# Performance work log

Hardware: AMD Instinct MI355X
Metric: run time of the kernel (lower is better)

## Reference

```python
import jax, jax.numpy as jnp
import numpy as np

BN_EPS = 1e-5

def setup_inputs() -> dict:
    key = jax.random.key(0)
    k0, k1, k2, k3, k4 = jax.random.split(key, 5)
    B, N, D, E = 8, 256, 128, 4096
    x_l = jax.random.normal(k0, (B, N, D), dtype=jnp.float32)
    src = jax.random.randint(k1, (E,), 0, N)
    dst = jax.random.randint(k2, (E,), 0, N)
    edge_index_l = jnp.stack([src, dst], axis=0)  # [2, E]
    mask_l = jax.random.randint(k3, (B, N), 0, 2).astype(bool)
    W = jax.random.normal(k4, (D, D), dtype=jnp.float32) * (1.0 / np.sqrt(D))
    b = jnp.zeros((D,), jnp.float32)
    gamma = jnp.ones((D,), jnp.float32)
    beta = jnp.zeros((D,), jnp.float32)
    return {"x_l": x_l, "edge_index_l": edge_index_l, "mask_l": mask_l,
            "W": W, "b": b, "gamma": gamma, "beta": beta}


def reference(x_l, edge_index_l, mask_l, W, b, gamma, beta):
    # x_l: [B, N, D]; edge_index_l: [2, E]; mask_l: [B, N] bool
    B, N, D = x_l.shape
    src, dst = edge_index_l[0], edge_index_l[1]
    # Vectorized replacement of the Python edge loop: edges with dst - src == 3
    # zero the mask at both endpoints (the explicit interaction zeroing in the
    # original is subsumed by the mask, since masked entries never survive).
    cov = (dst - src) == 3  # [E] bool
    hit = jnp.zeros((N,), bool)
    hit = hit.at[src].max(cov)
    hit = hit.at[dst].max(cov)
    mask = mask_l & ~hit[None, :]  # [B, N]
    # Pairwise mask: outer AND minus diagonal
    eye = jnp.eye(N, dtype=bool)
    pair_mask = (mask[:, :, None] & mask[:, None, :]) & ~eye[None]  # [B, N, N]
    # Outer-product interaction: [B, N, N, D]
    interaction = x_l[:, :, None, :] * x_l[:, None, :, :]
    # Linear
    h = jnp.einsum('bijd,ed->bije', interaction, W) + b
    # BatchNorm1d over the masked (selected) rows, training-mode batch stats.
    m = pair_mask[..., None].astype(h.dtype)  # [B, N, N, 1]
    cnt = jnp.maximum(jnp.sum(m), 1.0)
    mean = jnp.sum(h * m, axis=(0, 1, 2)) / cnt  # [D]
    var = jnp.sum(m * (h - mean) ** 2, axis=(0, 1, 2)) / cnt  # biased, as torch BN
    hn = (h - mean) * jax.lax.rsqrt(var + BN_EPS) * gamma + beta
    # Dropout is identity in eval mode; LeakyReLU slope 0.01 (torch default).
    out = jax.nn.leaky_relu(hn, negative_slope=0.01) * m  # zero non-selected entries
    return out, pair_mask
```

## Files before the change

### kernel.cpp

```cpp
#include <hip/hip_runtime.h>

#define B_ 8
#define N_ 256
#define D_ 128
#define E_ 4096

typedef __attribute__((ext_vector_type(8))) short bf16x8;
typedef __attribute__((ext_vector_type(4))) float f32x4;
typedef __attribute__((ext_vector_type(2))) float f32x2;

__device__ inline unsigned int pack2bf(float lo, float hi) {
    unsigned ul = __float_as_uint(lo);
    ul = ul + 0x7FFFu + ((ul >> 16) & 1u);
    unsigned uh = __float_as_uint(hi);
    uh = uh + 0x7FFFu + ((uh >> 16) & 1u);
    return (ul >> 16) | (uh & 0xFFFF0000u);
}

__device__ inline unsigned short f2bf(float f) {
    unsigned u = __float_as_uint(f);
    u = u + 0x7FFFu + ((u >> 16) & 1u);
    return (unsigned short)(u >> 16);
}


__global__ __launch_bounds__(256) void k_prep(const void* __restrict__ edges_raw,
                                              const void* __restrict__ mask_raw,
                                              const float* __restrict__ W,
                                              int* __restrict__ mask,
                                              int* __restrict__ jlist,
                                              int* __restrict__ jcnt,
                                              unsigned short* __restrict__ Wb,
                                              float* __restrict__ Wt,
                                              float* __restrict__ tq,
                                              float* __restrict__ dq) {
    int blk = blockIdx.x, tid = threadIdx.x;
    if (blk >= B_) {
        int idx = (blk - B_) * 256 + tid;
        if (idx < 16384) {
            float w = W[idx];
            Wb[idx] = f2bf(w);
            int e = idx >> 7, d = idx & 127;
            Wt[d * D_ + e] = w;
        } else if (idx < 16512) tq[idx - 16384] = 0.0f;
        else dq[idx - 16512] = 0.0f;
        return;
    }
    int b = blk;
    __shared__ unsigned char hit[N_];
    __shared__ int flags[2];
    __shared__ int wcnt[4], wbase[4];
    hit[tid] = 0;
    if (tid < 2) flags[tid] = 0;
    __syncthreads();

    const unsigned char* mb = (const unsigned char*)mask_raw;
    int loc_m = 0;
    for (int idx = tid; idx < B_ * N_; idx += 256)
        if ((idx & 3) && mb[idx]) loc_m = 1;
    if (loc_m) flags[0] = 1;
    const int* e32 = (const int*)edges_raw;
    int loc_e = 0;
    for (int idx = tid; idx < 2 * E_; idx += 256)
        if ((idx & 1) && e32[idx]) loc_e = 1;
    if (loc_e) flags[1] = 1;
    __syncthreads();

    int mask_is_u8 = flags[0], e_is_i32 = flags[1];
    const long long* e64 = (const long long*)edges_raw;
    for (int e = tid; e < E_; e += 256) {
        int s, d;
        if (e_is_i32) { s = e32[e]; d = e32[E_ + e]; }
        else          { s = (int)e64[e]; d = (int)e64[E_ + e]; }
        if (d - s == 3) { hit[s] = 1; hit[d] = 1; }
    }
    __syncthreads();

    const int* m32 = (const int*)mask_raw;
    int lane = tid & 63, wid = tid >> 6;
    int raw = mask_is_u8 ? (int)(mb[b * N_ + tid] != 0) : (int)(m32[b * N_ + tid] != 0);
    int m = raw && (hit[tid] == 0);
    mask[b * N_ + tid] = m;
    unsigned long long bal = __ballot(m);
    if (lane == 0) wcnt[wid] = __popcll(bal);
    __syncthreads();
    if (tid == 0) {
        int base = 0;
        for (int w = 0; w < 4; ++w) { wbase[w] = base; base += wcnt[w]; }
        jcnt[b] = base;
    }
    __syncthreads();
    if (m) {
        int pos = wbase[wid] + __popcll(bal & ((1ull << lane) - 1ull));
        jlist[b * N_ + pos] = tid;
    }
}

__global__ __launch_bounds__(128) void k_gram3(const float* __restrict__ x,
                                               const int* __restrict__ jlist,
                                               const int* __restrict__ jcnt,
                                               float* __restrict__ part,
                                               float* __restrict__ s1,
                                               float* __restrict__ cdiag) {
    int d = blockIdx.x, b = blockIdx.y, dp = threadIdx.x;
    int kc = jcnt[b];
    const int* jl = jlist + b * N_;
    const float* xb = x + (size_t)b * N_ * D_;
    float c0 = 0, c1 = 0, q0 = 0, q1 = 0, s0 = 0, s1a = 0;
    int t = 0;
    for (; t + 1 < kc; t += 2) {
        int i0 = jl[t], i1 = jl[t + 1];
        float xd0 = xb[i0 * D_ + d], xp0 = xb[i0 * D_ + dp];
        float xd1 = xb[i1 * D_ + d], xp1 = xb[i1 * D_ + dp];
        c0 += xd0 * xp0; q0 += (xd0 * xd0) * (xp0 * xp0); s0 += xd0;
        c1 += xd1 * xp1; q1 += (xd1 * xd1) * (xp1 * xp1); s1a += xd1;
    }
    if (t < kc) {
        int i0 = jl[t];
        float xd0 = xb[i0 * D_ + d], xp0 = xb[i0 * D_ + dp];
        c0 += xd0 * xp0; q0 += (xd0 * xd0) * (xp0 * xp0); s0 += xd0;
    }
    float c = c0 + c1, q = q0 + q1, sa = s0 + s1a;
    part[((size_t)b * D_ + d) * D_ + dp] = c * c - q;
    if (dp == d) cdiag[b * D_ + d] = c;
    if (dp == 0) s1[b * D_ + d] = sa;
}

__global__ __launch_bounds__(128) void k_mw2(const float* __restrict__ part,
                                             const float* __restrict__ Wt,
                                             const float* __restrict__ s1,
                                             const float* __restrict__ cdiag,
                                             float* __restrict__ tq,
                                             float* __restrict__ dq) {
    __shared__ float Ms[D_];
    __shared__ float svs;
    int d = blockIdx.x, e = threadIdx.x;
    float m = 0.0f;
#pragma unroll
    for (int b = 0; b < B_; ++b) m += part[((size_t)b * D_ + d) * D_ + e];
    Ms[e] = m;
    if (e == 0) {
        float sv = 0.0f;
#pragma unroll
        for (int b = 0; b < B_; ++b) {
            float s = s1[b * D_ + d];
            sv += s * s - cdiag[b * D_ + d];
        }
        svs = sv;
    }
    __syncthreads();
    float y = 0.0f;
#pragma unroll 8
    for (int p = 0; p < D_; ++p) y += Ms[p] * Wt[p * D_ + e];
    float wed = Wt[d * D_ + e];
    atomicAdd(tq + e, wed * y);
    atomicAdd(dq + e, wed * svs);
}

__global__ __launch_bounds__(256) void k_main(const float* __restrict__ x,
                                              const int* __restrict__ mask,
                                              const int* __restrict__ jlist,
                                              const int* __restrict__ jcnt,
                                              const unsigned short* __restrict__ Wb,
                                              const float* __restrict__ tq,
                                              const float* __restrict__ dq,
                                              const float* __restrict__ bvec,
                                              const float* __restrict__ gamma,
                                              const float* __restrict__ beta,
                                              float* __restrict__ out,
                                              float* __restrict__ pair) {
    __shared__ int msk[N_];
    __shared__ __align__(16) unsigned char Vsb[64 * 256];
    __shared__ float scs[D_], shs[D_];

    int b = blockIdx.y, i = blockIdx.x;
    int tid = threadIdx.x;
    msk[tid] = mask[b * N_ + tid];
    __syncthreads();
    int mi = msk[i];

    float pm = (mi && msk[tid] && tid != i) ? 1.0f : 0.0f;
    __builtin_nontemporal_store(pm, &pair[(size_t)(b * N_ + i) * N_ + tid]);

    f32x4 z4 = (f32x4)(0.f);
    f32x4* outrow = (f32x4*)(out + (size_t)(b * N_ + i) * N_ * D_);

    if (!mi) {
        for (int k = tid; k < N_ * D_ / 4; k += 256)
            __builtin_nontemporal_store(z4, &outrow[k]);
        return;
    }

    {
        int c = tid & 31, g = tid >> 5;
        for (int j = g; j < N_; j += 8)
            if (!msk[j] || j == i)
                __builtin_nontemporal_store(z4, &outrow[j * 32 + c]);
    }

    if (tid < D_) {
        float cnt = 0.0f;
#pragma unroll
        for (int bb = 0; bb < B_; ++bb) {
            float k = (float)jcnt[bb];
            cnt += k * k - k;
        }
        if (cnt < 1.0f) cnt = 1.0f;
        float be = bvec[tid];
        float mean = dq[tid] / cnt + be;
        float eh2 = tq[tid] / cnt + 2.0f * be * mean - be * be;
        float var = eh2 - mean * mean;
        if (var < 0.0f) var = 0.0f;
        float s = gamma[tid] * rsqrtf(var + 1e-5f);
        scs[tid] = s;
        shs[tid] = be * s + beta[tid] - mean * s;
    }

    int w = tid >> 6, l = tid & 63;
    int lo16 = l & 15, hi4 = l >> 4;
    int E0 = w * 32;

    bf16x8 bfrag[2][4];
#pragma unroll
    for (int et = 0; et < 2; ++et) {
        int e = E0 + 2 * lo16 + et;
#pragma unroll
        for (int ks = 0; ks < 4; ++ks)
            bfrag[et][ks] = *(const bf16x8*)(Wb + (size_t)e * D_ + ks * 32 + hi4 * 8);
    }

    int kc = jcnt[b];
    const int* jl = jlist + b * N_;
    const float* xi = x + (size_t)(b * N_ + i) * D_;
    float* outbase = out + (size_t)(b * N_ + i) * N_ * D_;

    for (int jt = 0; jt < kc; jt += 64) {
        __syncthreads();
        int jn = kc - jt; if (jn > 64) jn = 64;

        {
            int r = tid >> 2, q = tid & 3;
            int jrow = jt + r;
            bool ok = (r < jn);
            const float* xj = ok ? (x + (size_t)(b * N_ + jl[jrow]) * D_) : xi;
            int d0 = q * 32;
#pragma unroll
            for (int c4 = 0; c4 < 4; ++c4) {
                int d = d0 + c4 * 8;
                float4 a0 = *(const float4*)(xj + d);
                float4 a1 = *(const float4*)(xj + d + 4);
                float4 b0 = *(const float4*)(xi + d);
                float4 b1 = *(const float4*)(xi + d + 4);
                uint4 pk;
                pk.x = pack2bf(a0.x * b0.x, a0.y * b0.y);
                pk.y = pack2bf(a0.z * b0.z, a0.w * b0.w);
                pk.z = pack2bf(a1.x * b1.x, a1.y * b1.y);
                pk.w = pack2bf(a1.z * b1.z, a1.w * b1.w);
                if (!ok) pk = make_uint4(0u, 0u, 0u, 0u);
                int byte = r * 256 + ((d * 2) ^ ((r & 7) << 4));
                *(uint4*)(Vsb + byte) = pk;
            }
        }
        __syncthreads();

        f32x4 acc[4][2];
#pragma unroll
        for (int jq = 0; jq < 4; ++jq) {
            acc[jq][0] = (f32x4)(0.f);
            acc[jq][1] = (f32x4)(0.f);
            int rA = jq * 16 + lo16;
            int rbase = rA * 256;
            int rx = (rA & 7) << 4;
            bf16x8 a0 = *(const bf16x8*)(Vsb + rbase + (((hi4 * 8) * 2) ^ rx));
            bf16x8 a1 = *(const bf16x8*)(Vsb + rbase + (((32 + hi4 * 8) * 2) ^ rx));
            bf16x8 a2 = *(const bf16x8*)(Vsb + rbase + (((64 + hi4 * 8) * 2) ^ rx));
            bf16x8 a3 = *(const bf16x8*)(Vsb + rbase + (((96 + hi4 * 8) * 2) ^ rx));
            acc[jq][0] = __builtin_amdgcn_mfma_f32_16x16x32_bf16(a0, bfrag[0][0], acc[jq][0], 0, 0, 0);
            acc[jq][1] = __builtin_amdgcn_mfma_f32_16x16x32_bf16(a0, bfrag[1][0], acc[jq][1], 0, 0, 0);
            acc[jq][0] = __builtin_amdgcn_mfma_f32_16x16x32_bf16(a1, bfrag[0][1], acc[jq][0], 0, 0, 0);
            acc[jq][1] = __builtin_amdgcn_mfma_f32_16x16x32_bf16(a1, bfrag[1][1], acc[jq][1], 0, 0, 0);
            acc[jq][0] = __builtin_amdgcn_mfma_f32_16x16x32_bf16(a2, bfrag[0][2], acc[jq][0], 0, 0, 0);
            acc[jq][1] = __builtin_amdgcn_mfma_f32_16x16x32_bf16(a2, bfrag[1][2], acc[jq][1], 0, 0, 0);
            acc[jq][0] = __builtin_amdgcn_mfma_f32_16x16x32_bf16(a3, bfrag[0][3], acc[jq][0], 0, 0, 0);
            acc[jq][1] = __builtin_amdgcn_mfma_f32_16x16x32_bf16(a3, bfrag[1][3], acc[jq][1], 0, 0, 0);
        }

        float sc0 = scs[E0 + 2 * lo16], sh0 = shs[E0 + 2 * lo16];
        float sc1 = scs[E0 + 2 * lo16 + 1], sh1 = shs[E0 + 2 * lo16 + 1];
#pragma unroll
        for (int jq = 0; jq < 4; ++jq) {
#pragma unroll
            for (int v = 0; v < 4; ++v) {
                int jrow = jt + jq * 16 + hi4 * 4 + v;
                if (jrow < kc) {
                    int j = jl[jrow];
                    if (j != i) {
                        float h0 = acc[jq][0][v] * sc0 + sh0;
                        float h1 = acc[jq][1][v] * sc1 + sh1;
                        f32x2 o;
                        o.x = h0 >= 0.f ? h0 : 0.01f * h0;
                        o.y = h1 >= 0.f ? h1 : 0.01f * h1;
                        __builtin_nontemporal_store(o,
                            (f32x2*)(outbase + (size_t)j * D_ + E0 + 2 * lo16));
                    }
                }
            }
        }
    }
}

extern "C" void kernel_launch(void* const* d_in, const int* in_sizes, int n_in,
                              void* d_out, int out_size, void* d_ws, size_t ws_size,
                              hipStream_t stream) {
    const float* x = (const float*)d_in[0];
    const void* edges = d_in[1];
    const void* mask_in = d_in[2];
    const float* W = (const float*)d_in[3];
    const float* bvec = (const float*)d_in[4];
    const float* gamma = (const float*)d_in[5];
    const float* beta = (const float*)d_in[6];

    float* out = (float*)d_out;
    float* pair = out + (size_t)B_ * N_ * N_ * D_;

    char* ws = (char*)d_ws;
    int* mask = (int*)(ws + 0);
    int* jlist = (int*)(ws + 8192);
    int* jcnt = (int*)(ws + 16384);
    float* tq = (float*)(ws + 16448);
    float* dq = (float*)(ws + 16960);
    unsigned short* Wb = (unsigned short*)(ws + 17472);
    float* Wt = (float*)(ws + 50240);
    float* s1 = (float*)(ws + 115776);
    float* cdiag = (float*)(ws + 119872);
    float* part = (float*)(ws + 123968);

    k_prep<<<73, 256, 0, stream>>>(edges, mask_in, W, mask, jlist, jcnt, Wb, Wt, tq, dq);
    {
        dim3 g(D_, B_);
        k_gram3<<<g, 128, 0, stream>>>(x, jlist, jcnt, part, s1, cdiag);
    }
    k_mw2<<<128, 128, 0, stream>>>(part, Wt, s1, cdiag, tq, dq);
    {
        dim3 g(N_, B_);
        k_main<<<g, 256, 0, stream>>>(x, mask, jlist, jcnt, Wb, tq, dq,
                                      bvec, gamma, beta, out, pair);
    }
}
```

Baseline: 102.5 us.

## Build MFMA A-fragments directly in registers, drop LDS staging and barriers

Each wave now loads its own x_j rows from global memory, multiplies them by x_i held in registers, packs to bf16 and feeds the MFMA directly, so the shared-memory tile and the per-tile barriers are gone. Masked-out rows now skip the shared-mask load and write their zero pair row and output row with a fully unrolled store loop. The j index list is cached in LDS. In exchange, each of the four waves reloads and recomputes the same x_j products for its own slice of outputs, about four times the global loads and elementwise work.

```diff
diff --git a/kernel.cpp b/kernel.cpp
--- a/kernel.cpp
+++ b/kernel.cpp
@@ -170,33 +170,26 @@
                                               float* __restrict__ out,
                                               float* __restrict__ pair) {
     __shared__ int msk[N_];
-    __shared__ __align__(16) unsigned char Vsb[64 * 256];
+    __shared__ int jls[N_];
     __shared__ float scs[D_], shs[D_];
 
     int b = blockIdx.y, i = blockIdx.x;
     int tid = threadIdx.x;
-    msk[tid] = mask[b * N_ + tid];
-    __syncthreads();
-    int mi = msk[i];
-
-    float pm = (mi && msk[tid] && tid != i) ? 1.0f : 0.0f;
-    __builtin_nontemporal_store(pm, &pair[(size_t)(b * N_ + i) * N_ + tid]);
+    int mi = mask[b * N_ + i];
 
     f32x4 z4 = (f32x4)(0.f);
     f32x4* outrow = (f32x4*)(out + (size_t)(b * N_ + i) * N_ * D_);
 
     if (!mi) {
-        for (int k = tid; k < N_ * D_ / 4; k += 256)
-            __builtin_nontemporal_store(z4, &outrow[k]);
+        __builtin_nontemporal_store(0.0f, &pair[(size_t)(b * N_ + i) * N_ + tid]);
+#pragma unroll
+        for (int p = 0; p < 32; ++p)
+            __builtin_nontemporal_store(z4, &outrow[tid + 256 * p]);
         return;
     }
 
-    {
-        int c = tid & 31, g = tid >> 5;
-        for (int j = g; j < N_; j += 8)
-            if (!msk[j] || j == i)
-                __builtin_nontemporal_store(z4, &outrow[j * 32 + c]);
-    }
+    msk[tid] = mask[b * N_ + tid];
+    jls[tid] = jlist[b * N_ + tid];
 
     if (tid < D_) {
         float cnt = 0.0f;
@@ -215,11 +208,32 @@
         scs[tid] = s;
         shs[tid] = be * s + beta[tid] - mean * s;
     }
+    __syncthreads();
+
+    float pm = (msk[tid] && tid != i) ? 1.0f : 0.0f;
+    __builtin_nontemporal_store(pm, &pair[(size_t)(b * N_ + i) * N_ + tid]);
+
+    {
+        int c = tid & 31, g = tid >> 5;
+        for (int j = g; j < N_; j += 8)
+            if (!msk[j] || j == i)
+                __builtin_nontemporal_store(z4, &outrow[j * 32 + c]);
+    }
 
     int w = tid >> 6, l = tid & 63;
     int lo16 = l & 15, hi4 = l >> 4;
     int E0 = w * 32;
 
+    const float* xi = x + (size_t)(b * N_ + i) * D_;
+
+    float4 xi0[4], xi1[4];
+#pragma unroll
+    for (int ks = 0; ks < 4; ++ks) {
+        int d = ks * 32 + hi4 * 8;
+        xi0[ks] = *(const float4*)(xi + d);
+        xi1[ks] = *(const float4*)(xi + d + 4);
+    }
+
     bf16x8 bfrag[2][4];
 #pragma unroll
     for (int et = 0; et < 2; ++et) {
@@ -229,74 +243,45 @@
             bfrag[et][ks] = *(const bf16x8*)(Wb + (size_t)e * D_ + ks * 32 + hi4 * 8);
     }
 
+    float sc0 = scs[E0 + 2 * lo16], sh0 = shs[E0 + 2 * lo16];
+    float sc1 = scs[E0 + 2 * lo16 + 1], sh1 = shs[E0 + 2 * lo16 + 1];
+
     int kc = jcnt[b];
-    const int* jl = jlist + b * N_;
-    const float* xi = x + (size_t)(b * N_ + i) * D_;
+    const float* xb = x + (size_t)b * N_ * D_;
     float* outbase = out + (size_t)(b * N_ + i) * N_ * D_;
 
     for (int jt = 0; jt < kc; jt += 64) {
-        __syncthreads();
-        int jn = kc - jt; if (jn > 64) jn = 64;
-
-        {
-            int r = tid >> 2, q = tid & 3;
-            int jrow = jt + r;
-            bool ok = (r < jn);
-            const float* xj = ok ? (x + (size_t)(b * N_ + jl[jrow]) * D_) : xi;
-            int d0 = q * 32;
-#pragma unroll
-            for (int c4 = 0; c4 < 4; ++c4) {
-                int d = d0 + c4 * 8;
+#pragma unroll
+        for (int jq = 0; jq < 4; ++jq) {
+            int idx = jt + jq * 16 + lo16;
+            int cidx = idx < kc ? idx : kc - 1;
+            const float* xj = xb + (size_t)jls[cidx] * D_;
+
+            f32x4 acc0 = (f32x4)(0.f);
+            f32x4 acc1 = (f32x4)(0.f);
+#pragma unroll
+            for (int ks = 0; ks < 4; ++ks) {
+                int d = ks * 32 + hi4 * 8;
                 float4 a0 = *(const float4*)(xj + d);
                 float4 a1 = *(const float4*)(xj + d + 4);
-                float4 b0 = *(const float4*)(xi + d);
-                float4 b1 = *(const float4*)(xi + d + 4);
                 uint4 pk;
-                pk.x = pack2bf(a0.x * b0.x, a0.y * b0.y);
-                pk.y = pack2bf(a0.z * b0.z, a0.w * b0.w);
-                pk.z = pack2bf(a1.x * b1.x, a1.y * b1.y);
-                pk.w = pack2bf(a1.z * b1.z, a1.w * b1.w);
-                if (!ok) pk = make_uint4(0u, 0u, 0u, 0u);
-                int byte = r * 256 + ((d * 2) ^ ((r & 7) << 4));
-                *(uint4*)(Vsb + byte) = pk;
+                pk.x = pack2bf(a0.x * xi0[ks].x, a0.y * xi0[ks].y);
+                pk.y = pack2bf(a0.z * xi0[ks].z, a0.w * xi0[ks].w);
+                pk.z = pack2bf(a1.x * xi1[ks].x, a1.y * xi1[ks].y);
+                pk.w = pack2bf(a1.z * xi1[ks].z, a1.w * xi1[ks].w);
+                bf16x8 afr = *(bf16x8*)&pk;
+                acc0 = __builtin_amdgcn_mfma_f32_16x16x32_bf16(afr, bfrag[0][ks], acc0, 0, 0, 0);
+                acc1 = __builtin_amdgcn_mfma_f32_16x16x32_bf16(afr, bfrag[1][ks], acc1, 0, 0, 0);
             }
-        }
-        __syncthreads();
-
-        f32x4 acc[4][2];
-#pragma unroll
-        for (int jq = 0; jq < 4; ++jq) {
-            acc[jq][0] = (f32x4)(0.f);
-            acc[jq][1] = (f32x4)(0.f);
-            int rA = jq * 16 + lo16;
-            int rbase = rA * 256;
-            int rx = (rA & 7) << 4;
-            bf16x8 a0 = *(const bf16x8*)(Vsb + rbase + (((hi4 * 8) * 2) ^ rx));
-            bf16x8 a1 = *(const bf16x8*)(Vsb + rbase + (((32 + hi4 * 8) * 2) ^ rx));
-            bf16x8 a2 = *(const bf16x8*)(Vsb + rbase + (((64 + hi4 * 8) * 2) ^ rx));
-            bf16x8 a3 = *(const bf16x8*)(Vsb + rbase + (((96 + hi4 * 8) * 2) ^ rx));
-            acc[jq][0] = __builtin_amdgcn_mfma_f32_16x16x32_bf16(a0, bfrag[0][0], acc[jq][0], 0, 0, 0);
-            acc[jq][1] = __builtin_amdgcn_mfma_f32_16x16x32_bf16(a0, bfrag[1][0], acc[jq][1], 0, 0, 0);
-            acc[jq][0] = __builtin_amdgcn_mfma_f32_16x16x32_bf16(a1, bfrag[0][1], acc[jq][0], 0, 0, 0);
-            acc[jq][1] = __builtin_amdgcn_mfma_f32_16x16x32_bf16(a1, bfrag[1][1], acc[jq][1], 0, 0, 0);
-            acc[jq][0] = __builtin_amdgcn_mfma_f32_16x16x32_bf16(a2, bfrag[0][2], acc[jq][0], 0, 0, 0);
-            acc[jq][1] = __builtin_amdgcn_mfma_f32_16x16x32_bf16(a2, bfrag[1][2], acc[jq][1], 0, 0, 0);
-            acc[jq][0] = __builtin_amdgcn_mfma_f32_16x16x32_bf16(a3, bfrag[0][3], acc[jq][0], 0, 0, 0);
-            acc[jq][1] = __builtin_amdgcn_mfma_f32_16x16x32_bf16(a3, bfrag[1][3], acc[jq][1], 0, 0, 0);
-        }
-
-        float sc0 = scs[E0 + 2 * lo16], sh0 = shs[E0 + 2 * lo16];
-        float sc1 = scs[E0 + 2 * lo16 + 1], sh1 = shs[E0 + 2 * lo16 + 1];
-#pragma unroll
-        for (int jq = 0; jq < 4; ++jq) {
+
 #pragma unroll
             for (int v = 0; v < 4; ++v) {
                 int jrow = jt + jq * 16 + hi4 * 4 + v;
                 if (jrow < kc) {
-                    int j = jl[jrow];
+                    int j = jls[jrow];
                     if (j != i) {
-                        float h0 = acc[jq][0][v] * sc0 + sh0;
-                        float h1 = acc[jq][1][v] * sc1 + sh1;
+                        float h0 = acc0[v] * sc0 + sh0;
+                        float h1 = acc1[v] * sc1 + sh1;
                         f32x2 o;
                         o.x = h0 >= 0.f ? h0 : 0.01f * h0;
                         o.y = h1 >= 0.f ? h1 : 0.01f * h1;
```

New measurement: 113.2 us. 10.4% more time.
